# Kernel tuning notes

Measured on AMD Instinct MI355X. Metric: run time of the kernel, lower is better.

The kernel has to match this reference:

```python
import jax, jax.numpy as jnp
import numpy as np

L, S, N, E, H = 1024, 1024, 4, 1024, 16


def setup_inputs() -> dict:
    key = jax.random.key(0)
    ks = jax.random.split(key, 7)
    return {
        "query": jax.random.normal(ks[0], (L, N, E), jnp.float32),
        "key": jax.random.normal(ks[1], (S, N, E), jnp.float32),
        "value": jax.random.normal(ks[2], (S, N, E), jnp.float32),
        "in_proj_weight": jax.random.normal(ks[3], (3 * E, E), jnp.float32) * (E ** -0.5),
        "in_proj_bias": jax.random.normal(ks[4], (3 * E,), jnp.float32) * 0.02,
        "out_proj_weight": jax.random.normal(ks[5], (E, E), jnp.float32) * (E ** -0.5),
        "out_proj_bias": jax.random.normal(ks[6], (E,), jnp.float32) * 0.02,
        "num_heads": H,
    }


def _split_heads(x, n, h, hd):
    # (T, N, E) -> (N*h, T, hd), matching torch view(T, N*h, hd).transpose(0, 1)
    t = x.shape[0]
    return jnp.transpose(x.reshape(t, n * h, hd), (1, 0, 2))


def reference(query, key, value, in_proj_weight, in_proj_bias,
              out_proj_weight, out_proj_bias, num_heads):
    tgt_len, bsz, embed_dim = query.shape
    src_len = key.shape[0]
    head_dim = embed_dim // num_heads
    scaling = float(head_dim) ** -0.5

    # packed QKV projection (torch F.linear: x @ W.T + b), sliced as in source
    q = query @ in_proj_weight[:embed_dim].T + in_proj_bias[:embed_dim]
    k = key @ in_proj_weight[embed_dim:2 * embed_dim].T + in_proj_bias[embed_dim:2 * embed_dim]
    v = value @ in_proj_weight[2 * embed_dim:].T + in_proj_bias[2 * embed_dim:]
    q = q * scaling

    q = _split_heads(q, bsz, num_heads, head_dim)  # (N*H, L, hd)
    k = _split_heads(k, bsz, num_heads, head_dim)  # (N*H, S, hd)
    v = _split_heads(v, bsz, num_heads, head_dim)  # (N*H, S, hd)

    scores = jnp.einsum('bld,bsd->bls', q, k)           # (N*H, L, S)
    attn = jax.nn.softmax(scores, axis=-1)
    ctx = jnp.einsum('bls,bsd->bld', attn, v)           # (N*H, L, hd)

    # (N*H, L, hd) -> (L, N, E)
    ctx = jnp.transpose(ctx, (1, 0, 2)).reshape(tgt_len, bsz, embed_dim)
    attn_output = ctx @ out_proj_weight.T + out_proj_bias

    # need_weights=True path: average over heads -> (N, L, S)
    attn_weights = attn.reshape(bsz, num_heads, tgt_len, src_len).sum(axis=1) / num_heads
    return attn_output, attn_weights
```

## Files before the change

kernel.cpp:

```cpp
#include <hip/hip_runtime.h>

typedef unsigned short u16;
typedef __attribute__((ext_vector_type(8))) short short8;
typedef __attribute__((ext_vector_type(4))) float f32x4;

__device__ __forceinline__ u16 f2bf(float f) {
  unsigned int i = __float_as_uint(f);
  i += 0x7fffu + ((i >> 16) & 1u);
  return (u16)(i >> 16);
}

__device__ __forceinline__ short8 cvt8(const float* p) {
  float4 a = ((const float4*)p)[0];
  float4 b = ((const float4*)p)[1];
  short8 r;
  r[0] = (short)f2bf(a.x); r[1] = (short)f2bf(a.y);
  r[2] = (short)f2bf(a.z); r[3] = (short)f2bf(a.w);
  r[4] = (short)f2bf(b.x); r[5] = (short)f2bf(b.y);
  r[6] = (short)f2bf(b.z); r[7] = (short)f2bf(b.w);
  return r;
}

__global__ __launch_bounds__(256) void convert_bf16(
    const float* __restrict__ q, const float* __restrict__ k,
    const float* __restrict__ v, const float* __restrict__ Wi,
    const float* __restrict__ Wo,
    u16* __restrict__ qb, u16* __restrict__ kb, u16* __restrict__ vb,
    u16* __restrict__ Wib, u16* __restrict__ Wob)
{
  const float* src; u16* dst; int len8;
  switch (blockIdx.y) {
    case 0:  src = q;  dst = qb;  len8 = 524288; break;
    case 1:  src = k;  dst = kb;  len8 = 524288; break;
    case 2:  src = v;  dst = vb;  len8 = 524288; break;
    case 3:  src = Wi; dst = Wib; len8 = 393216; break;
    default: src = Wo; dst = Wob; len8 = 131072; break;
  }
  int stride = gridDim.x * 256;
  for (int i = blockIdx.x * 256 + threadIdx.x; i < len8; i += stride)
    *(short8*)(dst + (size_t)i * 8) = cvt8(src + (size_t)i * 8);
}

__global__ __launch_bounds__(256) void qkv_gemm(
    const u16* __restrict__ qb, const u16* __restrict__ kb,
    const u16* __restrict__ vb, const u16* __restrict__ W,
    const float* __restrict__ bias,
    u16* __restrict__ qh, u16* __restrict__ kh, u16* __restrict__ vt)
{
  __shared__ __align__(16) u16 SH[24576];

  const int tid  = threadIdx.x;
  const int wave = tid >> 6;
  const int lane = tid & 63;
  const int r    = lane & 15;
  const int q4   = lane >> 4;
  const int wm   = wave >> 1;
  const int wn   = wave & 1;

  const int orig = blockIdx.y * 24 + blockIdx.x;
  const int nid  = (orig & 7) * 96 + (orig >> 3);
  const int mt   = nid / 24;
  const int jt   = nid - mt * 24;
  const int src  = jt >> 3;
  const u16* X = (src == 0) ? qb : (src == 1) ? kb : vb;
  const int m0 = mt * 128;
  const int j0 = jt * 128;

  const int lrow = lane >> 2;
  const int lchk = ((lane & 3) ^ ((lane >> 3) & 3)) << 4;
  const char* Xc = (const char*)X;
  const char* Wc = (const char*)W;

  const int fchk = (q4 ^ ((r >> 1) & 3)) << 3;

  f32x4 acc[4][4];
  #pragma unroll
  for (int a = 0; a < 4; ++a)
    #pragma unroll
    for (int b = 0; b < 4; ++b)
      acc[a][b] = (f32x4){0.f, 0.f, 0.f, 0.f};

  auto STAGE = [&](int buf, int kt) {
    const int kbyte = kt * 64;
    u16* Ad = SH + buf * 4096;
    u16* Bd = SH + 12288 + buf * 4096;
    #pragma unroll
    for (int i = 0; i < 2; ++i) {
      const int g = wave * 2 + i;
      __builtin_amdgcn_global_load_lds(
          (const u16*)(Xc + (size_t)(m0 + g * 16 + lrow) * 2048 + kbyte + lchk),
          Ad + g * 512, 16, 0, 0);
      __builtin_amdgcn_global_load_lds(
          (const u16*)(Wc + (size_t)(j0 + g * 16 + lrow) * 2048 + kbyte + lchk),
          Bd + g * 512, 16, 0, 0);
    }
  };

  auto COMPUTE = [&](int cb) {
    const u16* As = SH + cb * 4096;
    const u16* Bs = SH + 12288 + cb * 4096;
    short8 af[4], bf[4];
    #pragma unroll
    for (int mi = 0; mi < 4; ++mi)
      af[mi] = *(const short8*)(&As[(wm * 64 + mi * 16 + r) * 32 + fchk]);
    #pragma unroll
    for (int ji = 0; ji < 4; ++ji)
      bf[ji] = *(const short8*)(&Bs[(wn * 64 + ji * 16 + r) * 32 + fchk]);
    #pragma unroll
    for (int mi = 0; mi < 4; ++mi)
      #pragma unroll
      for (int ji = 0; ji < 4; ++ji)
        acc[mi][ji] = __builtin_amdgcn_mfma_f32_16x16x32_bf16(af[mi], bf[ji], acc[mi][ji], 0, 0, 0);
  };

  STAGE(0, 0);
  STAGE(1, 1);
  int cb = 0;
  for (int kt = 0; kt < 31; ++kt) {
    asm volatile("s_waitcnt vmcnt(4) lgkmcnt(0)\n\ts_barrier" ::: "memory");
    if (kt < 30) {
      int nb = cb + 2; if (nb >= 3) nb -= 3;
      STAGE(nb, kt + 2);
    }
    COMPUTE(cb);
    if (++cb == 3) cb = 0;
  }
  asm volatile("s_waitcnt vmcnt(0) lgkmcnt(0)\n\ts_barrier" ::: "memory");
  COMPUTE(cb);

  __syncthreads();
  const int h0 = (j0 & 1023) >> 6;
  const int t0 = mt * 32;
  if (src < 2) {
    #pragma unroll
    for (int mi = 0; mi < 4; ++mi) {
      const int tt = wm * 16 + mi * 4 + q4;
      #pragma unroll
      for (int ji = 0; ji < 4; ++ji) {
        const int jj = wn * 64 + ji * 16 + r;
        const int dd = jj & 63, hq = jj >> 6;
        const int cs = (((dd >> 3) ^ (tt & 7)) << 3) + (dd & 7);
        #pragma unroll
        for (int rr = 0; rr < 4; ++rr) {
          float v = acc[mi][ji][rr] + bias[j0 + jj];
          SH[((rr * 2 + hq) * 32 + tt) * 64 + cs] =
              (src == 0) ? f2bf(v * 0.125f) : f2bf(v);
        }
      }
    }
    __syncthreads();
    u16* dst = (src == 0) ? qh : kh;
    #pragma unroll
    for (int c = 0; c < 8; ++c) {
      const int cid = c * 256 + tid;
      const int nn = cid >> 9, hq = (cid >> 8) & 1, tt = (cid >> 3) & 31, dc = cid & 7;
      short8 vv = *(const short8*)(SH + ((nn * 2 + hq) * 32 + tt) * 64 +
                                   ((dc ^ (tt & 7)) << 3));
      *(short8*)(dst + (size_t)(nn * 16 + h0 + hq) * 65536 +
                 (size_t)(t0 + tt) * 64 + dc * 8) = vv;
    }
  } else {
    #pragma unroll
    for (int mi = 0; mi < 4; ++mi) {
      const int tt = wm * 16 + mi * 4 + q4;
      const int tc = tt >> 3, toff = tt & 7;
      #pragma unroll
      for (int ji = 0; ji < 4; ++ji) {
        const int jj = wn * 64 + ji * 16 + r;
        const int dd = jj & 63, hq = jj >> 6;
        #pragma unroll
        for (int rr = 0; rr < 4; ++rr) {
          float v = acc[mi][ji][rr] + bias[j0 + jj];
          SH[((rr * 2 + hq) * 64 + dd) * 32 + ((tc ^ (dd & 3)) << 3) + toff] = f2bf(v);
        }
      }
    }
    __syncthreads();
    #pragma unroll
    for (int c = 0; c < 8; ++c) {
      const int cid = c * 256 + tid;
      const int bbv = cid >> 8, dd = (cid >> 2) & 63, tc = cid & 3;
      short8 vv = *(const short8*)(SH + (bbv * 64 + dd) * 32 +
                                   ((tc ^ (dd & 3)) << 3));
      const int bb = (bbv >> 1) * 16 + h0 + (bbv & 1);
      *(short8*)(vt + (size_t)bb * 65536 + (size_t)dd * 1024 + t0 + tc * 8) = vv;
    }
  }
}

__global__ __launch_bounds__(256) void attn_ctx_mfma(
    const u16* __restrict__ qh, const u16* __restrict__ kh,
    const u16* __restrict__ vt, u16* __restrict__ ctx,
    float* __restrict__ Zbuf)
{
  __shared__ __align__(16) u16 Ks[2][4096];
  __shared__ __align__(16) u16 Vs[2][4096];
  __shared__ __align__(16) u16 Pl[4][1024];

  const int tid = threadIdx.x;
  const int wv = tid >> 6, lane = tid & 63, r = lane & 15, q4 = lane >> 4;
  const int b  = blockIdx.y;
  const int lw = blockIdx.x * 64 + wv * 16;
  const int n = b >> 4, h = b & 15;

  const u16* qbase = qh + (size_t)b * 65536;
  const char* kc = (const char*)(kh + (size_t)b * 65536);
  const char* vc = (const char*)(vt + (size_t)b * 65536);
  u16* P = Pl[wv];

  const int ls  = lane >> 3;
  const int swzb = ((lane & 7) ^ ls) << 4;
  const int iw  = wv * 2;
  const size_t klo = (size_t)iw * 1024 + (size_t)ls * 128 + swzb;
  const size_t vlo = (size_t)iw * 16384 + (size_t)ls * 2048 + swzb;

  const int rsw = r & 7;
  const int c0 = (q4 ^ rsw) << 3;
  const int c1 = ((q4 ^ rsw) ^ 4) << 3;

  short8 aq0 = *(const short8*)(qbase + (size_t)(lw + r) * 64 + q4 * 8);
  short8 aq1 = *(const short8*)(qbase + (size_t)(lw + r) * 64 + 32 + q4 * 8);

  f32x4 oc[4];
  #pragma unroll
  for (int ji = 0; ji < 4; ++ji) oc[ji] = (f32x4){0.f, 0.f, 0.f, 0.f};
  float z[4] = {0.f, 0.f, 0.f, 0.f};

  {
    const char* kp = kc + klo;
    const char* vp = vc + vlo;
    u16* kd = &Ks[0][iw * 512];
    u16* vd = &Vs[0][iw * 512];
    __builtin_amdgcn_global_load_lds(kp,          kd,       16, 0, 0);
    __builtin_amdgcn_global_load_lds(kp + 1024,   kd + 512, 16, 0, 0);
    __builtin_amdgcn_global_load_lds(vp,          vd,       16, 0, 0);
    __builtin_amdgcn_global_load_lds(vp + 16384,  vd + 512, 16, 0, 0);
  }

  for (int it = 0; it < 16; ++it) {
    const int cur = it & 1;
    __syncthreads();
    const u16* Kb = Ks[cur];
    const u16* Vb = Vs[cur];

    f32x4 sc[4];
    #pragma unroll
    for (int ji = 0; ji < 4; ++ji) {
      const int row = (ji * 16 + r) * 64;
      short8 bk0 = *(const short8*)(Kb + row + c0);
      short8 bk1 = *(const short8*)(Kb + row + c1);
      f32x4 t = (f32x4){0.f, 0.f, 0.f, 0.f};
      t = __builtin_amdgcn_mfma_f32_16x16x32_bf16(aq0, bk0, t, 0, 0, 0);
      t = __builtin_amdgcn_mfma_f32_16x16x32_bf16(aq1, bk1, t, 0, 0, 0);
      sc[ji] = t;
    }

    if (it < 15) {
      const char* kp = kc + (size_t)(it + 1) * 8192 + klo;
      const char* vp = vc + (size_t)(it + 1) * 128  + vlo;
      u16* kd = &Ks[cur ^ 1][iw * 512];
      u16* vd = &Vs[cur ^ 1][iw * 512];
      __builtin_amdgcn_global_load_lds(kp,          kd,       16, 0, 0);
      __builtin_amdgcn_global_load_lds(kp + 1024,   kd + 512, 16, 0, 0);
      __builtin_amdgcn_global_load_lds(vp,          vd,       16, 0, 0);
      __builtin_amdgcn_global_load_lds(vp + 16384,  vd + 512, 16, 0, 0);
    }

    #pragma unroll
    for (int ji = 0; ji < 4; ++ji) {
      const int cw = ji * 2 + (r >> 3);
      #pragma unroll
      for (int rr = 0; rr < 4; ++rr) {
        float e = __expf(sc[ji][rr]);
        z[rr] += e;
        const int row = q4 * 4 + rr;
        P[row * 64 + ((cw ^ (row & 7)) << 3) + (r & 7)] = f2bf(e);
      }
    }
    asm volatile("s_waitcnt lgkmcnt(0)" ::: "memory");
    short8 ap0 = *(const short8*)(P + r * 64 + c0);
    short8 ap1 = *(const short8*)(P + r * 64 + c1);
    #pragma unroll
    for (int ji = 0; ji < 4; ++ji) {
      const int row = (ji * 16 + r) * 64;
      short8 bv0 = *(const short8*)(Vb + row + c0);
      short8 bv1 = *(const short8*)(Vb + row + c1);
      oc[ji] = __builtin_amdgcn_mfma_f32_16x16x32_bf16(ap0, bv0, oc[ji], 0, 0, 0);
      oc[ji] = __builtin_amdgcn_mfma_f32_16x16x32_bf16(ap1, bv1, oc[ji], 0, 0, 0);
    }
  }

  #pragma unroll
  for (int rr = 0; rr < 4; ++rr) {
    float zz = z[rr];
    zz += __shfl_xor(zz, 1);
    zz += __shfl_xor(zz, 2);
    zz += __shfl_xor(zz, 4);
    zz += __shfl_xor(zz, 8);
    z[rr] = zz;
  }

  #pragma unroll
  for (int rr = 0; rr < 4; ++rr) {
    float inv = 1.0f / z[rr];
    int l = lw + q4 * 4 + rr;
    u16* crow = ctx + ((size_t)l * 4 + n) * 1024 + h * 64;
    #pragma unroll
    for (int ji = 0; ji < 4; ++ji)
      crow[ji * 16 + r] = f2bf(oc[ji][rr] * inv);
    if (r == 0) Zbuf[(size_t)b * 1024 + l] = z[rr];
  }
}

__global__ __launch_bounds__(256) void attn_w_mfma(
    const u16* __restrict__ qh, const u16* __restrict__ kh,
    const float* __restrict__ Zbuf, float* __restrict__ out_w)
{
  __shared__ __align__(16) u16 Kw[2][4096];
  __shared__ float invZ[16][64];

  const int tid = threadIdx.x;
  const int wv = tid >> 6, lane = tid & 63, r = lane & 15, q4 = lane >> 4;
  const int lt = blockIdx.x;
  const int st = blockIdx.y;
  const int n  = blockIdx.z;
  const int l0 = lt * 64;
  const int s0 = st * 64;
  const int lw = l0 + wv * 16;

  const char* khc = (const char*)kh + (size_t)n * 2097152;

  const int ls  = lane >> 3;
  const int swzb = ((lane & 7) ^ ls) << 4;
  const int iw  = wv * 2;
  const size_t klo = (size_t)s0 * 128 + (size_t)iw * 1024 + (size_t)ls * 128 + swzb;

  const int rsw = r & 7;
  const int c0 = (q4 ^ rsw) << 3;
  const int c1 = ((q4 ^ rsw) ^ 4) << 3;

  for (int i = tid; i < 1024; i += 256) {
    int hh = i >> 6, row = i & 63;
    invZ[hh][row] = 1.0f / (Zbuf[(size_t)(n * 16 + hh) * 1024 + l0 + row] * 16.0f);
  }

  {
    const char* kp = khc + klo;
    u16* kd = &Kw[0][iw * 512];
    __builtin_amdgcn_global_load_lds(kp,        kd,       16, 0, 0);
    __builtin_amdgcn_global_load_lds(kp + 1024, kd + 512, 16, 0, 0);
  }
  const u16* q0 = qh + (size_t)(n * 16) * 65536;
  short8 aqc0 = *(const short8*)(q0 + (size_t)(lw + r) * 64 + q4 * 8);
  short8 aqc1 = *(const short8*)(q0 + (size_t)(lw + r) * 64 + 32 + q4 * 8);

  f32x4 wacc[4];
  #pragma unroll
  for (int ji = 0; ji < 4; ++ji) wacc[ji] = (f32x4){0.f, 0.f, 0.f, 0.f};

  for (int hh = 0; hh < 16; ++hh) {
    const int cur = hh & 1;
    __syncthreads();
    if (hh < 15) {
      const char* kp = khc + (size_t)(hh + 1) * 131072 + klo;
      u16* kd = &Kw[cur ^ 1][iw * 512];
      __builtin_amdgcn_global_load_lds(kp,        kd,       16, 0, 0);
      __builtin_amdgcn_global_load_lds(kp + 1024, kd + 512, 16, 0, 0);
    }
    const int hn = (hh < 15) ? hh + 1 : hh;
    const u16* qn = qh + (size_t)(n * 16 + hn) * 65536;
    short8 an0 = *(const short8*)(qn + (size_t)(lw + r) * 64 + q4 * 8);
    short8 an1 = *(const short8*)(qn + (size_t)(lw + r) * 64 + 32 + q4 * 8);

    const u16* Kb = Kw[cur];
    f32x4 sc[4];
    #pragma unroll
    for (int ji = 0; ji < 4; ++ji) {
      const int row = (ji * 16 + r) * 64;
      short8 bk0 = *(const short8*)(Kb + row + c0);
      short8 bk1 = *(const short8*)(Kb + row + c1);
      f32x4 t = (f32x4){0.f, 0.f, 0.f, 0.f};
      t = __builtin_amdgcn_mfma_f32_16x16x32_bf16(aqc0, bk0, t, 0, 0, 0);
      t = __builtin_amdgcn_mfma_f32_16x16x32_bf16(aqc1, bk1, t, 0, 0, 0);
      sc[ji] = t;
    }
    #pragma unroll
    for (int rr = 0; rr < 4; ++rr) {
      float iv = invZ[hh][wv * 16 + q4 * 4 + rr];
      #pragma unroll
      for (int ji = 0; ji < 4; ++ji)
        wacc[ji][rr] += __expf(sc[ji][rr]) * iv;
    }
    aqc0 = an0; aqc1 = an1;
  }

  #pragma unroll
  for (int ji = 0; ji < 4; ++ji)
    #pragma unroll
    for (int rr = 0; rr < 4; ++rr) {
      int row = lw + q4 * 4 + rr;
      int col = s0 + ji * 16 + r;
      out_w[(size_t)n * 1048576 + (size_t)row * 1024 + col] = wacc[ji][rr];
    }
}

__global__ __launch_bounds__(256) void out_gemm(
    const u16* __restrict__ ctx, const u16* __restrict__ W,
    const float* __restrict__ bias, float* __restrict__ out)
{
  __shared__ __align__(16) u16 SH[18432];

  const int tid  = threadIdx.x;
  const int wave = tid >> 6;
  const int lane = tid & 63;
  const int r    = lane & 15;
  const int q4   = lane >> 4;
  const int wm   = wave >> 1;
  const int wn   = wave & 1;

  const int orig = blockIdx.y * 16 + blockIdx.x;
  const int nid  = (orig & 7) * 64 + (orig >> 3);
  const int mt   = nid >> 4;
  const int jt   = nid & 15;
  const int m0 = mt * 128;
  const int j0 = jt * 64;

  const int lrow = lane >> 2;
  const int lchk = ((lane & 3) ^ ((lane >> 3) & 3)) << 4;
  const char* Ac = (const char*)ctx;
  const char* Wc = (const char*)W;
  const int fchk = (q4 ^ ((r >> 1) & 3)) << 3;

  f32x4 acc[4][2];
  #pragma unroll
  for (int a = 0; a < 4; ++a)
    #pragma unroll
    for (int b = 0; b < 2; ++b)
      acc[a][b] = (f32x4){0.f, 0.f, 0.f, 0.f};

  auto STAGE = [&](int buf, int kt) {
    const int kbyte = kt * 64;
    u16* Ad = SH + buf * 4096;
    u16* Bd = SH + 12288 + buf * 2048;
    #pragma unroll
    for (int i = 0; i < 2; ++i) {
      const int g = wave * 2 + i;
      __builtin_amdgcn_global_load_lds(
          (const u16*)(Ac + (size_t)(m0 + g * 16 + lrow) * 2048 + kbyte + lchk),
          Ad + g * 512, 16, 0, 0);
    }
    __builtin_amdgcn_global_load_lds(
        (const u16*)(Wc + (size_t)(j0 + wave * 16 + lrow) * 2048 + kbyte + lchk),
        Bd + wave * 512, 16, 0, 0);
  };

  auto COMPUTE = [&](int cb) {
    const u16* As = SH + cb * 4096;
    const u16* Bs = SH + 12288 + cb * 2048;
    short8 af[4], bf[2];
    #pragma unroll
    for (int mi = 0; mi < 4; ++mi)
      af[mi] = *(const short8*)(&As[(wm * 64 + mi * 16 + r) * 32 + fchk]);
    #pragma unroll
    for (int ji = 0; ji < 2; ++ji)
      bf[ji] = *(const short8*)(&Bs[(wn * 32 + ji * 16 + r) * 32 + fchk]);
    #pragma unroll
    for (int mi = 0; mi < 4; ++mi)
      #pragma unroll
      for (int ji = 0; ji < 2; ++ji)
        acc[mi][ji] = __builtin_amdgcn_mfma_f32_16x16x32_bf16(af[mi], bf[ji], acc[mi][ji], 0, 0, 0);
  };

  STAGE(0, 0);
  STAGE(1, 1);
  int cb = 0;
  for (int kt = 0; kt < 31; ++kt) {
    asm volatile("s_waitcnt vmcnt(3) lgkmcnt(0)\n\ts_barrier" ::: "memory");
    if (kt < 30) {
      int nb = cb + 2; if (nb >= 3) nb -= 3;
      STAGE(nb, kt + 2);
    }
    COMPUTE(cb);
    if (++cb == 3) cb = 0;
  }
  asm volatile("s_waitcnt vmcnt(0) lgkmcnt(0)\n\ts_barrier" ::: "memory");
  COMPUTE(cb);

  #pragma unroll
  for (int mi = 0; mi < 4; ++mi) {
    #pragma unroll
    for (int ji = 0; ji < 2; ++ji) {
      #pragma unroll
      for (int rr = 0; rr < 4; ++rr) {
        int m = m0 + wm * 64 + mi * 16 + q4 * 4 + rr;
        int j = j0 + wn * 32 + ji * 16 + r;
        out[(size_t)m * 1024 + j] = acc[mi][ji][rr] + bias[j];
      }
    }
  }
}

extern "C" void kernel_launch(void* const* d_in, const int* in_sizes, int n_in,
                              void* d_out, int out_size, void* d_ws, size_t ws_size,
                              hipStream_t stream) {
  const float* query = (const float*)d_in[0];
  const float* key   = (const float*)d_in[1];
  const float* value = (const float*)d_in[2];
  const float* W_in  = (const float*)d_in[3];
  const float* b_in  = (const float*)d_in[4];
  const float* W_out = (const float*)d_in[5];
  const float* b_out = (const float*)d_in[6];
  float* out = (float*)d_out;

  u16* qb  = (u16*)d_ws;
  u16* kb  = qb  + (size_t)4194304;
  u16* vb  = kb  + (size_t)4194304;
  u16* Wib = vb  + (size_t)4194304;
  u16* Wob = Wib + (size_t)3145728;
  u16* qh  = Wob + (size_t)1048576;
  u16* kh  = qh  + (size_t)4194304;
  u16* vt  = kh  + (size_t)4194304;
  u16* ctx = vt  + (size_t)4194304;
  float* Zbuf = (float*)(ctx + (size_t)4194304);

  convert_bf16<<<dim3(512, 5), 256, 0, stream>>>(query, key, value, W_in, W_out,
                                                 qb, kb, vb, Wib, Wob);
  qkv_gemm<<<dim3(24, 32), 256, 0, stream>>>(qb, kb, vb, Wib, b_in, qh, kh, vt);
  attn_ctx_mfma<<<dim3(16, 64), 256, 0, stream>>>(qh, kh, vt, ctx, Zbuf);
  attn_w_mfma<<<dim3(16, 16, 4), 256, 0, stream>>>(qh, kh, Zbuf, out + (size_t)4194304);
  out_gemm<<<dim3(16, 32), 256, 0, stream>>>(ctx, Wob, b_out, out);
}
```

Baseline: 232.4 us.

## Merge attention-weights and output-projection kernels into one launch

The head-averaged attention weights kernel and the output projection GEMM are now a single kernel whose grid is partitioned by block index: the first 512 blocks run the out-projection GEMM and the remaining 1024 compute attention weights. Both stages depend only on earlier kernels, so running them concurrently removes one launch and lets the compute-heavy weight blocks fill the GPU alongside the GEMM tail. The trade-off is that both branches share one shared-memory allocation and register budget, which may lower occupancy for the lighter branch.

Result: faster. 224.6 us (-3.4%).

```diff
diff --git a/kernel.cpp b/kernel.cpp
--- a/kernel.cpp
+++ b/kernel.cpp
@@ -70,7 +70,6 @@
   const int lchk = ((lane & 3) ^ ((lane >> 3) & 3)) << 4;
   const char* Xc = (const char*)X;
   const char* Wc = (const char*)W;
-
   const int fchk = (q4 ^ ((r >> 1) & 3)) << 3;
 
   f32x4 acc[4][4];
@@ -312,191 +311,187 @@
   }
 }
 
-__global__ __launch_bounds__(256) void attn_w_mfma(
+__global__ __launch_bounds__(256) void tail_fused(
     const u16* __restrict__ qh, const u16* __restrict__ kh,
-    const float* __restrict__ Zbuf, float* __restrict__ out_w)
-{
-  __shared__ __align__(16) u16 Kw[2][4096];
-  __shared__ float invZ[16][64];
-
-  const int tid = threadIdx.x;
-  const int wv = tid >> 6, lane = tid & 63, r = lane & 15, q4 = lane >> 4;
-  const int lt = blockIdx.x;
-  const int st = blockIdx.y;
-  const int n  = blockIdx.z;
-  const int l0 = lt * 64;
-  const int s0 = st * 64;
-  const int lw = l0 + wv * 16;
-
-  const char* khc = (const char*)kh + (size_t)n * 2097152;
-
-  const int ls  = lane >> 3;
-  const int swzb = ((lane & 7) ^ ls) << 4;
-  const int iw  = wv * 2;
-  const size_t klo = (size_t)s0 * 128 + (size_t)iw * 1024 + (size_t)ls * 128 + swzb;
-
-  const int rsw = r & 7;
-  const int c0 = (q4 ^ rsw) << 3;
-  const int c1 = ((q4 ^ rsw) ^ 4) << 3;
-
-  for (int i = tid; i < 1024; i += 256) {
-    int hh = i >> 6, row = i & 63;
-    invZ[hh][row] = 1.0f / (Zbuf[(size_t)(n * 16 + hh) * 1024 + l0 + row] * 16.0f);
-  }
-
-  {
-    const char* kp = khc + klo;
-    u16* kd = &Kw[0][iw * 512];
-    __builtin_amdgcn_global_load_lds(kp,        kd,       16, 0, 0);
-    __builtin_amdgcn_global_load_lds(kp + 1024, kd + 512, 16, 0, 0);
-  }
-  const u16* q0 = qh + (size_t)(n * 16) * 65536;
-  short8 aqc0 = *(const short8*)(q0 + (size_t)(lw + r) * 64 + q4 * 8);
-  short8 aqc1 = *(const short8*)(q0 + (size_t)(lw + r) * 64 + 32 + q4 * 8);
-
-  f32x4 wacc[4];
-  #pragma unroll
-  for (int ji = 0; ji < 4; ++ji) wacc[ji] = (f32x4){0.f, 0.f, 0.f, 0.f};
-
-  for (int hh = 0; hh < 16; ++hh) {
-    const int cur = hh & 1;
-    __syncthreads();
-    if (hh < 15) {
-      const char* kp = khc + (size_t)(hh + 1) * 131072 + klo;
-      u16* kd = &Kw[cur ^ 1][iw * 512];
-      __builtin_amdgcn_global_load_lds(kp,        kd,       16, 0, 0);
-      __builtin_amdgcn_global_load_lds(kp + 1024, kd + 512, 16, 0, 0);
-    }
-    const int hn = (hh < 15) ? hh + 1 : hh;
-    const u16* qn = qh + (size_t)(n * 16 + hn) * 65536;
-    short8 an0 = *(const short8*)(qn + (size_t)(lw + r) * 64 + q4 * 8);
-    short8 an1 = *(const short8*)(qn + (size_t)(lw + r) * 64 + 32 + q4 * 8);
-
-    const u16* Kb = Kw[cur];
-    f32x4 sc[4];
-    #pragma unroll
-    for (int ji = 0; ji < 4; ++ji) {
-      const int row = (ji * 16 + r) * 64;
-      short8 bk0 = *(const short8*)(Kb + row + c0);
-      short8 bk1 = *(const short8*)(Kb + row + c1);
-      f32x4 t = (f32x4){0.f, 0.f, 0.f, 0.f};
-      t = __builtin_amdgcn_mfma_f32_16x16x32_bf16(aqc0, bk0, t, 0, 0, 0);
-      t = __builtin_amdgcn_mfma_f32_16x16x32_bf16(aqc1, bk1, t, 0, 0, 0);
-      sc[ji] = t;
-    }
-    #pragma unroll
-    for (int rr = 0; rr < 4; ++rr) {
-      float iv = invZ[hh][wv * 16 + q4 * 4 + rr];
-      #pragma unroll
-      for (int ji = 0; ji < 4; ++ji)
-        wacc[ji][rr] += __expf(sc[ji][rr]) * iv;
-    }
-    aqc0 = an0; aqc1 = an1;
-  }
-
-  #pragma unroll
-  for (int ji = 0; ji < 4; ++ji)
-    #pragma unroll
-    for (int rr = 0; rr < 4; ++rr) {
-      int row = lw + q4 * 4 + rr;
-      int col = s0 + ji * 16 + r;
-      out_w[(size_t)n * 1048576 + (size_t)row * 1024 + col] = wacc[ji][rr];
-    }
-}
-
-__global__ __launch_bounds__(256) void out_gemm(
+    const float* __restrict__ Zbuf, float* __restrict__ out_w,
     const u16* __restrict__ ctx, const u16* __restrict__ W,
     const float* __restrict__ bias, float* __restrict__ out)
 {
   __shared__ __align__(16) u16 SH[18432];
 
-  const int tid  = threadIdx.x;
-  const int wave = tid >> 6;
-  const int lane = tid & 63;
-  const int r    = lane & 15;
-  const int q4   = lane >> 4;
-  const int wm   = wave >> 1;
-  const int wn   = wave & 1;
-
-  const int orig = blockIdx.y * 16 + blockIdx.x;
-  const int nid  = (orig & 7) * 64 + (orig >> 3);
-  const int mt   = nid >> 4;
-  const int jt   = nid & 15;
-  const int m0 = mt * 128;
-  const int j0 = jt * 64;
-
-  const int lrow = lane >> 2;
-  const int lchk = ((lane & 3) ^ ((lane >> 3) & 3)) << 4;
-  const char* Ac = (const char*)ctx;
-  const char* Wc = (const char*)W;
-  const int fchk = (q4 ^ ((r >> 1) & 3)) << 3;
-
-  f32x4 acc[4][2];
-  #pragma unroll
-  for (int a = 0; a < 4; ++a)
-    #pragma unroll
-    for (int b = 0; b < 2; ++b)
-      acc[a][b] = (f32x4){0.f, 0.f, 0.f, 0.f};
-
-  auto STAGE = [&](int buf, int kt) {
-    const int kbyte = kt * 64;
-    u16* Ad = SH + buf * 4096;
-    u16* Bd = SH + 12288 + buf * 2048;
-    #pragma unroll
-    for (int i = 0; i < 2; ++i) {
-      const int g = wave * 2 + i;
+  const int tid = threadIdx.x;
+  const int wv = tid >> 6, lane = tid & 63, r = lane & 15, q4 = lane >> 4;
+
+  if (blockIdx.x < 512) {
+    const int wave = wv;
+    const int wm   = wave >> 1;
+    const int wn   = wave & 1;
+    const int orig = blockIdx.x;
+    const int nid  = (orig & 7) * 64 + (orig >> 3);
+    const int mt   = nid >> 4;
+    const int jt   = nid & 15;
+    const int m0 = mt * 128;
+    const int j0 = jt * 64;
+
+    const int lrow = lane >> 2;
+    const int lchk = ((lane & 3) ^ ((lane >> 3) & 3)) << 4;
+    const char* Ac = (const char*)ctx;
+    const char* Wc = (const char*)W;
+    const int fchk = (q4 ^ ((r >> 1) & 3)) << 3;
+
+    f32x4 acc[4][2];
+    #pragma unroll
+    for (int a = 0; a < 4; ++a)
+      #pragma unroll
+      for (int b = 0; b < 2; ++b)
+        acc[a][b] = (f32x4){0.f, 0.f, 0.f, 0.f};
+
+    auto STAGE = [&](int buf, int kt) {
+      const int kbyte = kt * 64;
+      u16* Ad = SH + buf * 4096;
+      u16* Bd = SH + 12288 + buf * 2048;
+      #pragma unroll
+      for (int i = 0; i < 2; ++i) {
+        const int g = wave * 2 + i;
+        __builtin_amdgcn_global_load_lds(
+            (const u16*)(Ac + (size_t)(m0 + g * 16 + lrow) * 2048 + kbyte + lchk),
+            Ad + g * 512, 16, 0, 0);
+      }
       __builtin_amdgcn_global_load_lds(
-          (const u16*)(Ac + (size_t)(m0 + g * 16 + lrow) * 2048 + kbyte + lchk),
-          Ad + g * 512, 16, 0, 0);
-    }
-    __builtin_amdgcn_global_load_lds(
-        (const u16*)(Wc + (size_t)(j0 + wave * 16 + lrow) * 2048 + kbyte + lchk),
-        Bd + wave * 512, 16, 0, 0);
-  };
-
-  auto COMPUTE = [&](int cb) {
-    const u16* As = SH + cb * 4096;
-    const u16* Bs = SH + 12288 + cb * 2048;
-    short8 af[4], bf[2];
-    #pragma unroll
-    for (int mi = 0; mi < 4; ++mi)
-      af[mi] = *(const short8*)(&As[(wm * 64 + mi * 16 + r) * 32 + fchk]);
-    #pragma unroll
-    for (int ji = 0; ji < 2; ++ji)
-      bf[ji] = *(const short8*)(&Bs[(wn * 32 + ji * 16 + r) * 32 + fchk]);
-    #pragma unroll
-    for (int mi = 0; mi < 4; ++mi)
+          (const u16*)(Wc + (size_t)(j0 + wave * 16 + lrow) * 2048 + kbyte + lchk),
+          Bd + wave * 512, 16, 0, 0);
+    };
+
+    auto COMPUTE = [&](int cb) {
+      const u16* As = SH + cb * 4096;
+      const u16* Bs = SH + 12288 + cb * 2048;
+      short8 af[4], bf[2];
+      #pragma unroll
+      for (int mi = 0; mi < 4; ++mi)
+        af[mi] = *(const short8*)(&As[(wm * 64 + mi * 16 + r) * 32 + fchk]);
       #pragma unroll
       for (int ji = 0; ji < 2; ++ji)
-        acc[mi][ji] = __builtin_amdgcn_mfma_f32_16x16x32_bf16(af[mi], bf[ji], acc[mi][ji], 0, 0, 0);
-  };
-
-  STAGE(0, 0);
-  STAGE(1, 1);
-  int cb = 0;
-  for (int kt = 0; kt < 31; ++kt) {
-    asm volatile("s_waitcnt vmcnt(3) lgkmcnt(0)\n\ts_barrier" ::: "memory");
-    if (kt < 30) {
-      int nb = cb + 2; if (nb >= 3) nb -= 3;
-      STAGE(nb, kt + 2);
-    }
+        bf[ji] = *(const short8*)(&Bs[(wn * 32 + ji * 16 + r) * 32 + fchk]);
+      #pragma unroll
+      for (int mi = 0; mi < 4; ++mi)
+        #pragma unroll
+        for (int ji = 0; ji < 2; ++ji)
+          acc[mi][ji] = __builtin_amdgcn_mfma_f32_16x16x32_bf16(af[mi], bf[ji], acc[mi][ji], 0, 0, 0);
+    };
+
+    STAGE(0, 0);
+    STAGE(1, 1);
+    int cb = 0;
+    for (int kt = 0; kt < 31; ++kt) {
+      asm volatile("s_waitcnt vmcnt(3) lgkmcnt(0)\n\ts_barrier" ::: "memory");
+      if (kt < 30) {
+        int nb = cb + 2; if (nb >= 3) nb -= 3;
+        STAGE(nb, kt + 2);
+      }
+      COMPUTE(cb);
+      if (++cb == 3) cb = 0;
+    }
+    asm volatile("s_waitcnt vmcnt(0) lgkmcnt(0)\n\ts_barrier" ::: "memory");
     COMPUTE(cb);
-    if (++cb == 3) cb = 0;
-  }
-  asm volatile("s_waitcnt vmcnt(0) lgkmcnt(0)\n\ts_barrier" ::: "memory");
-  COMPUTE(cb);
-
-  #pragma unroll
-  for (int mi = 0; mi < 4; ++mi) {
-    #pragma unroll
-    for (int ji = 0; ji < 2; ++ji) {
+
+    #pragma unroll
+    for (int mi = 0; mi < 4; ++mi) {
+      #pragma unroll
+      for (int ji = 0; ji < 2; ++ji) {
+        #pragma unroll
+        for (int rr = 0; rr < 4; ++rr) {
+          int m = m0 + wm * 64 + mi * 16 + q4 * 4 + rr;
+          int j = j0 + wn * 32 + ji * 16 + r;
+          out[(size_t)m * 1024 + j] = acc[mi][ji][rr] + bias[j];
+        }
+      }
+    }
+  } else {
+    const int id2 = blockIdx.x - 512;
+    const int lt = id2 & 15;
+    const int st = (id2 >> 4) & 15;
+    const int n  = id2 >> 8;
+    const int l0 = lt * 64;
+    const int s0 = st * 64;
+    const int lw = l0 + wv * 16;
+
+    u16* Kw = SH;
+    float* invZ = (float*)(SH + 8192);
+
+    const char* khc = (const char*)kh + (size_t)n * 2097152;
+
+    const int ls  = lane >> 3;
+    const int swzb = ((lane & 7) ^ ls) << 4;
+    const int iw  = wv * 2;
+    const size_t klo = (size_t)s0 * 128 + (size_t)iw * 1024 + (size_t)ls * 128 + swzb;
+
+    const int rsw = r & 7;
+    const int c0 = (q4 ^ rsw) << 3;
+    const int c1 = ((q4 ^ rsw) ^ 4) << 3;
+
+    for (int i = tid; i < 1024; i += 256) {
+      int hh = i >> 6, row = i & 63;
+      invZ[hh * 64 + row] = 1.0f / (Zbuf[(size_t)(n * 16 + hh) * 1024 + l0 + row] * 16.0f);
+    }
+
+    {
+      const char* kp = khc + klo;
+      u16* kd = &Kw[iw * 512];
+      __builtin_amdgcn_global_load_lds(kp,        kd,       16, 0, 0);
+      __builtin_amdgcn_global_load_lds(kp + 1024, kd + 512, 16, 0, 0);
+    }
+    const u16* q0 = qh + (size_t)(n * 16) * 65536;
+    short8 aqc0 = *(const short8*)(q0 + (size_t)(lw + r) * 64 + q4 * 8);
+    short8 aqc1 = *(const short8*)(q0 + (size_t)(lw + r) * 64 + 32 + q4 * 8);
+
+    f32x4 wacc[4];
+    #pragma unroll
+    for (int ji = 0; ji < 4; ++ji) wacc[ji] = (f32x4){0.f, 0.f, 0.f, 0.f};
+
+    for (int hh = 0; hh < 16; ++hh) {
+      const int cur = hh & 1;
+      __syncthreads();
+      if (hh < 15) {
+        const char* kp = khc + (size_t)(hh + 1) * 131072 + klo;
+        u16* kd = &Kw[(cur ^ 1) * 4096 + iw * 512];
+        __builtin_amdgcn_global_load_lds(kp,        kd,       16, 0, 0);
+        __builtin_amdgcn_global_load_lds(kp + 1024, kd + 512, 16, 0, 0);
+      }
+      const int hn = (hh < 15) ? hh + 1 : hh;
+      const u16* qn = qh + (size_t)(n * 16 + hn) * 65536;
+      short8 an0 = *(const short8*)(qn + (size_t)(lw + r) * 64 + q4 * 8);
+      short8 an1 = *(const short8*)(qn + (size_t)(lw + r) * 64 + 32 + q4 * 8);
+
+      const u16* Kb = Kw + cur * 4096;
+      f32x4 sc[4];
+      #pragma unroll
+      for (int ji = 0; ji < 4; ++ji) {
+        const int row = (ji * 16 + r) * 64;
+        short8 bk0 = *(const short8*)(Kb + row + c0);
+        short8 bk1 = *(const short8*)(Kb + row + c1);
+        f32x4 t = (f32x4){0.f, 0.f, 0.f, 0.f};
+        t = __builtin_amdgcn_mfma_f32_16x16x32_bf16(aqc0, bk0, t, 0, 0, 0);
+        t = __builtin_amdgcn_mfma_f32_16x16x32_bf16(aqc1, bk1, t, 0, 0, 0);
+        sc[ji] = t;
+      }
       #pragma unroll
       for (int rr = 0; rr < 4; ++rr) {
-        int m = m0 + wm * 64 + mi * 16 + q4 * 4 + rr;
-        int j = j0 + wn * 32 + ji * 16 + r;
-        out[(size_t)m * 1024 + j] = acc[mi][ji][rr] + bias[j];
-      }
-    }
+        float iv = invZ[hh * 64 + wv * 16 + q4 * 4 + rr];
+        #pragma unroll
+        for (int ji = 0; ji < 4; ++ji)
+          wacc[ji][rr] += __expf(sc[ji][rr]) * iv;
+      }
+      aqc0 = an0; aqc1 = an1;
+    }
+
+    #pragma unroll
+    for (int ji = 0; ji < 4; ++ji)
+      #pragma unroll
+      for (int rr = 0; rr < 4; ++rr) {
+        int row = lw + q4 * 4 + rr;
+        int col = s0 + ji * 16 + r;
+        out_w[(size_t)n * 1048576 + (size_t)row * 1024 + col] = wacc[ji][rr];
+      }
   }
 }
 
@@ -527,6 +522,6 @@
                                                  qb, kb, vb, Wib, Wob);
   qkv_gemm<<<dim3(24, 32), 256, 0, stream>>>(qb, kb, vb, Wib, b_in, qh, kh, vt);
   attn_ctx_mfma<<<dim3(16, 64), 256, 0, stream>>>(qh, kh, vt, ctx, Zbuf);
-  attn_w_mfma<<<dim3(16, 16, 4), 256, 0, stream>>>(qh, kh, Zbuf, out + (size_t)4194304);
-  out_gemm<<<dim3(16, 32), 256, 0, stream>>>(ctx, Wob, b_out, out);
-}
+  tail_fused<<<dim3(1536), 256, 0, stream>>>(qh, kh, Zbuf, out + (size_t)4194304,
+                                             ctx, Wob, b_out, out);
+}
```
